# Performance work log

Measured on AMD Instinct MI355X. Metric: run time of the kernel, lower is better.

Reference implementation:

```python
import jax, jax.numpy as jnp
import numpy as np

N = 256                     # num_nodes
P = N * (N - 1) // 2        # undirected pairs (32640)
B = 32                      # batch size
H = 64                      # hidden_dim

# edge ordering matches the torch loops: for i<j append [i,j] then [j,i]
_iu = np.triu_indices(N, 1)
SRC_P = jnp.asarray(_iu[0])                                   # (P,) pair src i
DST_P = jnp.asarray(_iu[1])                                   # (P,) pair dst j
SRC_D = jnp.asarray(np.stack([_iu[0], _iu[1]], 1).ravel())    # (2P,) directed src, interleaved
DST_D = jnp.asarray(np.stack([_iu[1], _iu[0]], 1).ravel())    # (2P,) directed dst
# GCNConv adds self-loops internally
SRC_F = jnp.concatenate([SRC_D, jnp.arange(N)])               # (2P+N,)
DST_F = jnp.concatenate([DST_D, jnp.arange(N)])


def _glorot(key, fan_in, fan_out):
    s = (2.0 / (fan_in + fan_out)) ** 0.5
    return jax.random.normal(key, (fan_in, fan_out), dtype=jnp.float32) * s


def setup_inputs() -> dict:
    key = jax.random.key(0)
    ks = jax.random.split(key, 8)
    # edge decisions in {0, 0.5, 1}; one-hot current-edge indicator
    dec = jax.random.choice(ks[0], jnp.array([0.0, 0.5, 1.0], dtype=jnp.float32), (B, P))
    cur = jax.random.randint(ks[1], (B,), 0, P)
    ind = jax.nn.one_hot(cur, P, dtype=jnp.float32)
    x = jnp.concatenate([dec, ind], axis=1)                   # (B, 2P)
    return {
        "x": x,
        "W1": _glorot(ks[2], 3, H), "b1": jnp.zeros((H,), jnp.float32),
        "W2": _glorot(ks[3], H, H), "b2": jnp.zeros((H,), jnp.float32),
        "W3": _glorot(ks[4], H, H), "b3": jnp.zeros((H,), jnp.float32),
        "We1": _glorot(ks[5], 2 * H + 3, H), "be1": jnp.zeros((H,), jnp.float32),
        "We2": _glorot(ks[6], H, 1), "be2": jnp.zeros((1,), jnp.float32),
    }


def _gcn_conv(h, W, b, norm):
    # h: (B, N, Fin) -> (B, N, Fout); symmetric-normalized gather-scatter over
    # the complete graph + self loops (all GCN degrees equal N here).
    hw = h @ W                                                # (B, N, Fout)
    msg = hw[:, SRC_F, :] * norm[None, :, None]               # (B, 2P+N, Fout)
    agg = jnp.zeros_like(hw).at[:, DST_F, :].add(msg)         # scatter-add
    return agg + b


def reference(x, W1, b1, W2, b2, W3, b3, We1, be1, We2, be2):
    dec = x[:, :P]                                            # (B, P) edge decisions
    ind = x[:, P:]                                            # (B, P) current-edge indicator

    # per-pair edge features, duplicated for both directed copies (interleaved)
    ef = jnp.stack([(dec == 1.0).astype(x.dtype),
                    (dec != 0.5).astype(x.dtype),
                    ind], axis=-1)                            # (B, P, 3)
    ea = jnp.repeat(ef, 2, axis=1)                            # (B, 2P, 3)

    # node degrees under the decided adjacency (decision == 1 pairs)
    a_rep = jnp.repeat((dec == 1.0).astype(x.dtype), 2, axis=1)   # (B, 2P)
    deg = jnp.zeros((x.shape[0], N), x.dtype).at[:, DST_D].add(a_rep)

    cur = jnp.argmax(ind, axis=1)                             # (B,)
    i_node = SRC_P[cur]
    j_node = DST_P[cur]
    bidx = jnp.arange(x.shape[0])
    attached = (jnp.zeros((x.shape[0], N), x.dtype)
                .at[bidx, i_node].set(1.0)
                .at[bidx, j_node].set(1.0))

    node_feat = jnp.stack([deg / (N - 1),
                           (deg == 0.0).astype(x.dtype),
                           attached], axis=-1)                # (B, N, 3)

    # GCN normalization on complete graph + self loops: every degree == N
    deg_gcn = jnp.zeros((N,), x.dtype).at[DST_F].add(1.0)
    norm = jax.lax.rsqrt(deg_gcn[SRC_F] * deg_gcn[DST_F])     # (2P+N,), all 1/N

    h = jax.nn.relu(_gcn_conv(node_feat, W1, b1, norm))
    h = jax.nn.relu(_gcn_conv(h, W2, b2, norm))
    h = jax.nn.relu(_gcn_conv(h, W3, b3, norm))               # (B, N, H)

    # edge head: gather endpoints + edge attrs -> MLP
    rep = jnp.concatenate([h[:, SRC_D, :], h[:, DST_D, :], ea], axis=-1)  # (B, 2P, 2H+3)
    hm = jax.nn.relu(rep @ We1 + be1)
    logits = (hm @ We2 + be2)[..., 0]                         # (B, 2P)

    # select the two directed copies of the current edge (fixed-shape mask)
    sel = jnp.stack([2 * cur, 2 * cur + 1], axis=1)           # (B, 2)
    return jax.nn.sigmoid(jnp.take_along_axis(logits, sel, axis=1))
```

## Files before the change

### kernel.cpp

```cpp
#include <hip/hip_runtime.h>
#include <math.h>

#define NN 256
#define PP 32640
#define HH 64
#define BB 32
#define NF4 (PP / 4)

__global__ __launch_bounds__(1024) void gnn_fused(
    const float* __restrict__ x,
    const float* __restrict__ W1, const float* __restrict__ b1,
    const float* __restrict__ W2, const float* __restrict__ b2,
    const float* __restrict__ W3, const float* __restrict__ b3,
    const float* __restrict__ We1, const float* __restrict__ be1,
    const float* __restrict__ We2, const float* __restrict__ be2,
    float* __restrict__ out)
{
    const int b    = blockIdx.x;
    const int tid  = threadIdx.x;
    const int lane = tid & 63;
    const int w    = tid >> 6;

    __shared__ unsigned char touched[NN];
    __shared__ float gS[HH];
    __shared__ float pr[4][HH];
    __shared__ int   s_cur, s_cnt, s_pop;

    if (tid < NN) touched[tid] = 0;
    if (tid == 0) { s_cur = 0; s_cnt = 0; s_pop = 0; }
    __syncthreads();

    const float*  decp = x + (size_t)b * (2 * PP);
    const float4* dec4 = (const float4*)decp;
    const float4* ind4 = (const float4*)(decp + PP);

    int cnt = 0;
    for (int q = tid; q < NF4; q += 1024) {
        float4 d  = dec4[q];
        float4 iv = ind4[q];
        const int p0 = q * 4;

        int i = (int)((511.0f - sqrtf(261121.0f - 8.0f * (float)p0)) * 0.5f);
        while (i * (511 - i) / 2 > p0) --i;
        while ((i + 1) * (510 - i) / 2 <= p0) ++i;
        int rowStart = i * (511 - i) / 2;

        float dv[4]  = {d.x, d.y, d.z, d.w};
        float ivv[4] = {iv.x, iv.y, iv.z, iv.w};
        #pragma unroll
        for (int u = 0; u < 4; ++u) {
            const int p = p0 + u;
            while (p - rowStart >= 255 - i) { ++i; rowStart = i * (511 - i) / 2; }
            if (ivv[u] > 0.5f) s_cur = p;
            if (dv[u] == 1.0f) {
                const int j = i + 1 + (p - rowStart);
                touched[i] = 1;
                touched[j] = 1;
                ++cnt;
            }
        }
    }

    #pragma unroll
    for (int off = 32; off > 0; off >>= 1) cnt += __shfl_down(cnt, off);
    if (lane == 0) atomicAdd(&s_cnt, cnt);
    __syncthreads();

    if (tid < NN) {
        unsigned long long m = __ballot(touched[tid] != 0);
        if (lane == 0) atomicAdd(&s_pop, __popcll(m));
    }
    __syncthreads();

    const float f0 = (float)(2 * s_cnt) * (1.0f / 255.0f);
    const float f1 = (float)(NN - s_pop);

    if (tid < HH) {
        float s = f0 * W1[tid] + f1 * W1[HH + tid] + 2.0f * W1[2 * HH + tid];
        gS[tid] = fmaxf(s * (1.0f / 256.0f) + b1[tid], 0.0f);
    }
    __syncthreads();

    if (tid < 256) {
        float s = 0.0f;
        const float* Wp = W2 + (w * 16) * HH + lane;
        #pragma unroll
        for (int kk = 0; kk < 16; ++kk) s += gS[w * 16 + kk] * Wp[kk * HH];
        pr[w][lane] = s;
    }
    __syncthreads();
    if (tid < HH)
        gS[tid] = fmaxf(pr[0][tid] + pr[1][tid] + pr[2][tid] + pr[3][tid] + b2[tid], 0.0f);
    __syncthreads();

    if (tid < 256) {
        float s = 0.0f;
        const float* Wp = W3 + (w * 16) * HH + lane;
        #pragma unroll
        for (int kk = 0; kk < 16; ++kk) s += gS[w * 16 + kk] * Wp[kk * HH];
        pr[w][lane] = s;
    }
    __syncthreads();
    if (tid < HH)
        gS[tid] = fmaxf(pr[0][tid] + pr[1][tid] + pr[2][tid] + pr[3][tid] + b3[tid], 0.0f);
    __syncthreads();

    if (tid < 256) {
        float s = 0.0f;
        const float* Wa = We1 + (w * 16) * HH + lane;
        const float* Wb = We1 + (64 + w * 16) * HH + lane;
        #pragma unroll
        for (int kk = 0; kk < 16; ++kk)
            s += gS[w * 16 + kk] * (Wa[kk * HH] + Wb[kk * HH]);
        pr[w][lane] = s;
    }
    __syncthreads();
    if (tid < HH) {
        const float dcur = decp[s_cur];
        const float e0 = (dcur == 1.0f) ? 1.0f : 0.0f;
        const float e1 = (dcur != 0.5f) ? 1.0f : 0.0f;
        float v = pr[0][tid] + pr[1][tid] + pr[2][tid] + pr[3][tid] + be1[tid]
                + e0 * We1[128 * HH + tid] + e1 * We1[129 * HH + tid]
                + We1[130 * HH + tid];
        v = fmaxf(v, 0.0f);

        float contrib = v * We2[tid];
        #pragma unroll
        for (int off = 32; off > 0; off >>= 1)
            contrib += __shfl_down(contrib, off);

        if (tid == 0) {
            const float sig = 1.0f / (1.0f + expf(-(contrib + be2[0])));
            out[b * 2 + 0] = sig;
            out[b * 2 + 1] = sig;
        }
    }
}

extern "C" void kernel_launch(void* const* d_in, const int* in_sizes, int n_in,
                              void* d_out, int out_size, void* d_ws, size_t ws_size,
                              hipStream_t stream) {
    const float* x   = (const float*)d_in[0];
    const float* W1  = (const float*)d_in[1];
    const float* b1  = (const float*)d_in[2];
    const float* W2  = (const float*)d_in[3];
    const float* b2  = (const float*)d_in[4];
    const float* W3  = (const float*)d_in[5];
    const float* b3  = (const float*)d_in[6];
    const float* We1 = (const float*)d_in[7];
    const float* be1 = (const float*)d_in[8];
    const float* We2 = (const float*)d_in[9];
    const float* be2 = (const float*)d_in[10];
    float* out = (float*)d_out;

    gnn_fused<<<BB, 1024, 0, stream>>>(x, W1, b1, W2, b2, W3, b3,
                                       We1, be1, We2, be2, out);
}
```

Before: 15.24 us.

## Split per-batch scan across 8 blocks with cooperative grid sync

Replaces the 32-block, 1024-thread kernel with a cooperative launch of 256 blocks of 256 threads, each scanning one eighth of a batch row. Per-chunk touched-node bitmasks, edge counts and the current-edge decision go to workspace, and after a grid-wide sync the first 32 blocks merge them and run the small MLP chain. MLP weights are prefetched into registers before the grid sync so their loads overlap the wait. The aim is to spread the memory-bound scan over more CUs, at the cost of a grid barrier and cooperative launch overhead.

Measured after the change: 42.79 us. +180.7%, slower.

```diff
diff --git a/kernel.cpp b/kernel.cpp
--- a/kernel.cpp
+++ b/kernel.cpp
@@ -1,33 +1,47 @@
 #include <hip/hip_runtime.h>
+#include <hip/hip_cooperative_groups.h>
 #include <math.h>
+
+namespace cg = cooperative_groups;
 
 #define NN 256
 #define PP 32640
 #define HH 64
 #define BB 32
+#define NBLK 256
+#define CPB 8
 #define NF4 (PP / 4)
-
-__global__ __launch_bounds__(1024) void gnn_fused(
+#define F4B (NF4 / CPB)
+
+__global__ __launch_bounds__(256) void gnn_coop(
     const float* __restrict__ x,
     const float* __restrict__ W1, const float* __restrict__ b1,
     const float* __restrict__ W2, const float* __restrict__ b2,
     const float* __restrict__ W3, const float* __restrict__ b3,
     const float* __restrict__ We1, const float* __restrict__ be1,
     const float* __restrict__ We2, const float* __restrict__ be2,
+    unsigned int* __restrict__ ws_mask,
+    int* __restrict__ ws_cnt,
+    float* __restrict__ ws_dcur,
     float* __restrict__ out)
 {
-    const int b    = blockIdx.x;
+    const int blk  = blockIdx.x;
     const int tid  = threadIdx.x;
     const int lane = tid & 63;
     const int w    = tid >> 6;
 
     __shared__ unsigned char touched[NN];
+    __shared__ int   wcnt4[4];
+    __shared__ unsigned int mw[64];
+    __shared__ int   ic[CPB];
     __shared__ float gS[HH];
     __shared__ float pr[4][HH];
-    __shared__ int   s_cur, s_cnt, s_pop;
-
-    if (tid < NN) touched[tid] = 0;
-    if (tid == 0) { s_cur = 0; s_cnt = 0; s_pop = 0; }
+    __shared__ int   s_pop;
+
+    const int b     = blk >> 3;
+    const int chunk = blk & 7;
+
+    touched[tid] = 0;
     __syncthreads();
 
     const float*  decp = x + (size_t)b * (2 * PP);
@@ -35,7 +49,8 @@
     const float4* ind4 = (const float4*)(decp + PP);
 
     int cnt = 0;
-    for (int q = tid; q < NF4; q += 1024) {
+    for (int qq = tid; qq < F4B; qq += 256) {
+        const int q  = chunk * F4B + qq;
         float4 d  = dec4[q];
         float4 iv = ind4[q];
         const int p0 = q * 4;
@@ -51,7 +66,7 @@
         for (int u = 0; u < 4; ++u) {
             const int p = p0 + u;
             while (p - rowStart >= 255 - i) { ++i; rowStart = i * (511 - i) / 2; }
-            if (ivv[u] > 0.5f) s_cur = p;
+            if (ivv[u] > 0.5f) ws_dcur[b] = dv[u];
             if (dv[u] == 1.0f) {
                 const int j = i + 1 + (p - rowStart);
                 touched[i] = 1;
@@ -60,79 +75,120 @@
             }
         }
     }
-
-    #pragma unroll
-    for (int off = 32; off > 0; off >>= 1) cnt += __shfl_down(cnt, off);
-    if (lane == 0) atomicAdd(&s_cnt, cnt);
     __syncthreads();
 
-    if (tid < NN) {
+    {
         unsigned long long m = __ballot(touched[tid] != 0);
-        if (lane == 0) atomicAdd(&s_pop, __popcll(m));
-    }
-    __syncthreads();
-
-    const float f0 = (float)(2 * s_cnt) * (1.0f / 255.0f);
-    const float f1 = (float)(NN - s_pop);
-
-    if (tid < HH) {
-        float s = f0 * W1[tid] + f1 * W1[HH + tid] + 2.0f * W1[2 * HH + tid];
-        gS[tid] = fmaxf(s * (1.0f / 256.0f) + b1[tid], 0.0f);
-    }
-    __syncthreads();
-
-    if (tid < 256) {
-        float s = 0.0f;
-        const float* Wp = W2 + (w * 16) * HH + lane;
-        #pragma unroll
-        for (int kk = 0; kk < 16; ++kk) s += gS[w * 16 + kk] * Wp[kk * HH];
-        pr[w][lane] = s;
-    }
-    __syncthreads();
-    if (tid < HH)
-        gS[tid] = fmaxf(pr[0][tid] + pr[1][tid] + pr[2][tid] + pr[3][tid] + b2[tid], 0.0f);
-    __syncthreads();
-
-    if (tid < 256) {
-        float s = 0.0f;
-        const float* Wp = W3 + (w * 16) * HH + lane;
-        #pragma unroll
-        for (int kk = 0; kk < 16; ++kk) s += gS[w * 16 + kk] * Wp[kk * HH];
-        pr[w][lane] = s;
-    }
-    __syncthreads();
-    if (tid < HH)
-        gS[tid] = fmaxf(pr[0][tid] + pr[1][tid] + pr[2][tid] + pr[3][tid] + b3[tid], 0.0f);
-    __syncthreads();
-
-    if (tid < 256) {
-        float s = 0.0f;
-        const float* Wa = We1 + (w * 16) * HH + lane;
-        const float* Wb = We1 + (64 + w * 16) * HH + lane;
-        #pragma unroll
-        for (int kk = 0; kk < 16; ++kk)
-            s += gS[w * 16 + kk] * (Wa[kk * HH] + Wb[kk * HH]);
-        pr[w][lane] = s;
-    }
-    __syncthreads();
-    if (tid < HH) {
-        const float dcur = decp[s_cur];
-        const float e0 = (dcur == 1.0f) ? 1.0f : 0.0f;
-        const float e1 = (dcur != 0.5f) ? 1.0f : 0.0f;
-        float v = pr[0][tid] + pr[1][tid] + pr[2][tid] + pr[3][tid] + be1[tid]
-                + e0 * We1[128 * HH + tid] + e1 * We1[129 * HH + tid]
-                + We1[130 * HH + tid];
-        v = fmaxf(v, 0.0f);
-
-        float contrib = v * We2[tid];
-        #pragma unroll
-        for (int off = 32; off > 0; off >>= 1)
-            contrib += __shfl_down(contrib, off);
-
-        if (tid == 0) {
-            const float sig = 1.0f / (1.0f + expf(-(contrib + be2[0])));
-            out[b * 2 + 0] = sig;
-            out[b * 2 + 1] = sig;
+        if (lane == 0) {
+            ws_mask[blk * 8 + w * 2 + 0] = (unsigned int)m;
+            ws_mask[blk * 8 + w * 2 + 1] = (unsigned int)(m >> 32);
+        }
+        #pragma unroll
+        for (int off = 32; off > 0; off >>= 1) cnt += __shfl_down(cnt, off);
+        if (lane == 0) wcnt4[w] = cnt;
+        __syncthreads();
+        if (tid == 0) ws_cnt[blk] = wcnt4[0] + wcnt4[1] + wcnt4[2] + wcnt4[3];
+    }
+
+    float w2r[16], w3r[16], war[16], wbr[16];
+    float w1r0 = 0, w1r1 = 0, w1r2 = 0, b1r = 0, b2r = 0, b3r = 0, be1r = 0;
+    float er0 = 0, er1 = 0, er2 = 0, we2r = 0, be2r = 0;
+    if (blk < BB) {
+        #pragma unroll
+        for (int kk = 0; kk < 16; ++kk) {
+            w2r[kk] = W2 [(w * 16 + kk) * HH + lane];
+            w3r[kk] = W3 [(w * 16 + kk) * HH + lane];
+            war[kk] = We1[(w * 16 + kk) * HH + lane];
+            wbr[kk] = We1[(64 + w * 16 + kk) * HH + lane];
+        }
+        if (tid < HH) {
+            w1r0 = W1[tid]; w1r1 = W1[HH + tid]; w1r2 = W1[2 * HH + tid];
+            b1r = b1[tid]; b2r = b2[tid]; b3r = b3[tid]; be1r = be1[tid];
+            er0 = We1[128 * HH + tid]; er1 = We1[129 * HH + tid];
+            er2 = We1[130 * HH + tid]; we2r = We2[tid];
+        }
+        be2r = be2[0];
+    }
+
+    cg::this_grid().sync();
+
+    if (blk < BB) {
+        const int eb = blk;
+        const float dcur = ws_dcur[eb];
+
+        if (tid == 0) s_pop = 0;
+        if (tid < 64) mw[tid] = ws_mask[eb * 64 + tid];
+        if (tid < CPB) ic[tid] = ws_cnt[eb * CPB + tid];
+        __syncthreads();
+
+        if (tid < 8) {
+            unsigned int o = 0;
+            #pragma unroll
+            for (int c = 0; c < CPB; ++c) o |= mw[c * 8 + tid];
+            atomicAdd(&s_pop, __popc(o));
+        }
+        __syncthreads();
+
+        int scnt = 0;
+        #pragma unroll
+        for (int c = 0; c < CPB; ++c) scnt += ic[c];
+
+        const float f0 = (float)(2 * scnt) * (1.0f / 255.0f);
+        const float f1 = (float)(NN - s_pop);
+
+        if (tid < HH) {
+            float s = f0 * w1r0 + f1 * w1r1 + 2.0f * w1r2;
+            gS[tid] = fmaxf(s * (1.0f / 256.0f) + b1r, 0.0f);
+        }
+        __syncthreads();
+
+        {
+            float s = 0.0f;
+            #pragma unroll
+            for (int kk = 0; kk < 16; ++kk) s += gS[w * 16 + kk] * w2r[kk];
+            pr[w][lane] = s;
+        }
+        __syncthreads();
+        if (tid < HH)
+            gS[tid] = fmaxf(pr[0][tid] + pr[1][tid] + pr[2][tid] + pr[3][tid] + b2r, 0.0f);
+        __syncthreads();
+
+        {
+            float s = 0.0f;
+            #pragma unroll
+            for (int kk = 0; kk < 16; ++kk) s += gS[w * 16 + kk] * w3r[kk];
+            pr[w][lane] = s;
+        }
+        __syncthreads();
+        if (tid < HH)
+            gS[tid] = fmaxf(pr[0][tid] + pr[1][tid] + pr[2][tid] + pr[3][tid] + b3r, 0.0f);
+        __syncthreads();
+
+        {
+            float s = 0.0f;
+            #pragma unroll
+            for (int kk = 0; kk < 16; ++kk)
+                s += gS[w * 16 + kk] * (war[kk] + wbr[kk]);
+            pr[w][lane] = s;
+        }
+        __syncthreads();
+        if (tid < HH) {
+            const float e0 = (dcur == 1.0f) ? 1.0f : 0.0f;
+            const float e1 = (dcur != 0.5f) ? 1.0f : 0.0f;
+            float v = pr[0][tid] + pr[1][tid] + pr[2][tid] + pr[3][tid] + be1r
+                    + e0 * er0 + e1 * er1 + er2;
+            v = fmaxf(v, 0.0f);
+
+            float contrib = v * we2r;
+            #pragma unroll
+            for (int off = 32; off > 0; off >>= 1)
+                contrib += __shfl_down(contrib, off);
+
+            if (tid == 0) {
+                const float sig = 1.0f / (1.0f + expf(-(contrib + be2r)));
+                out[eb * 2 + 0] = sig;
+                out[eb * 2 + 1] = sig;
+            }
         }
     }
 }
@@ -153,6 +209,16 @@
     const float* be2 = (const float*)d_in[10];
     float* out = (float*)d_out;
 
-    gnn_fused<<<BB, 1024, 0, stream>>>(x, W1, b1, W2, b2, W3, b3,
-                                       We1, be1, We2, be2, out);
+    unsigned int* ws_mask = (unsigned int*)d_ws;
+    int*   ws_cnt  = (int*)(ws_mask + (size_t)NBLK * 8);
+    float* ws_dcur = (float*)(ws_cnt + NBLK);
+
+    void* args[] = {
+        (void*)&x, (void*)&W1, (void*)&b1, (void*)&W2, (void*)&b2,
+        (void*)&W3, (void*)&b3, (void*)&We1, (void*)&be1, (void*)&We2,
+        (void*)&be2, (void*)&ws_mask, (void*)&ws_cnt, (void*)&ws_dcur,
+        (void*)&out
+    };
+    hipLaunchCooperativeKernel((const void*)gnn_coop, dim3(NBLK), dim3(256),
+                               args, 0, stream);
 }
```
